# Kernel optimization log

Measured on AMD Instinct MI355X. Metric: run time of the kernel, lower is better.

The kernel has to match this reference:

```python
import jax, jax.numpy as jnp
import numpy as np

PARALLISM = 128          # Subarray[0]
O_BITS = 8               # ADC_resolution
SCALE = float(2 ** O_BITS - 1)          # 255.0
MAXCURRENT = 0.02 * PARALLISM           # 2.56 ; a_scale/w_scale == 2**32-1 so guards skip them


def setup_inputs() -> dict:
    key = jax.random.key(0)
    k1, k2, k3 = jax.random.split(key, 3)
    B, K, N = 8192, 4096, 4096
    x = jax.random.normal(k1, (B, K), dtype=jnp.float32) * 0.1
    weight = jax.random.normal(k2, (N, K), dtype=jnp.float32)  # torch Linear layout [out, in]
    bias = jax.random.normal(k3, (N,), dtype=jnp.float32)
    return {"x": x, "weight": weight, "bias": bias, "layer": 1}


def _quantize_partial(x):
    # output_quantize.forward: clamp to +/-maxcurrent, scale to [−scale, scale], round (STE), rescale
    y = jnp.clip(x, -MAXCURRENT, MAXCURRENT)
    y = y / MAXCURRENT * SCALE
    y = y + jax.lax.stop_gradient(jnp.round(y) - y)  # Round.apply with straight-through grad
    return y / SCALE * MAXCURRENT


def reference(x, weight, bias, layer):
    # Hard_fc: chunked VMM along the input-feature (row) dim with per-subarray ADC quantization
    B, K = x.shape
    w = weight.T                      # [K, N]
    N = w.shape[1]
    num = K // PARALLISM              # K chosen divisible by PARALLISM (32 chunks)
    xc = x.reshape(B, num, PARALLISM).swapaxes(0, 1)       # [num, B, P]
    wc = w.reshape(num, PARALLISM, N)                       # [num, P, N]

    def step(acc, chunk):
        xi, wi = chunk                # [B, P], [P, N]
        return acc + _quantize_partial(xi @ wi), None

    acc0 = jnp.zeros((B, N), dtype=x.dtype)
    out, _ = jax.lax.scan(step, acc0, (xc, wc))
    out = out + bias
    return out.reshape(B, -1)
```

## Files before the change

### kernel.cpp

```cpp
#include <hip/hip_runtime.h>


typedef __attribute__((ext_vector_type(8))) short short8;
typedef __attribute__((ext_vector_type(8))) unsigned short ushort8;
typedef __attribute__((ext_vector_type(4))) float floatx4;

#define BM 128
#define BN 128
#define BK 64

static __device__ __forceinline__ unsigned short f2bf(float f) {
    union { float f; unsigned int u; } v; v.f = f;
    unsigned int u = v.u;
    unsigned int r = (u + 0x7fffu + ((u >> 16) & 1u)) >> 16;
    return (unsigned short)r;
}

__global__ void cast_kernel(const float* __restrict__ in,
                            unsigned short* __restrict__ out,
                            long n8, float s) {
    long i = (long)blockIdx.x * 256 + threadIdx.x;
    const long stride = (long)gridDim.x * 256;
    for (; i < n8; i += stride) {
        float4 a = ((const float4*)in)[2 * i];
        float4 b = ((const float4*)in)[2 * i + 1];
        ushort8 o;
        o[0] = f2bf(a.x * s); o[1] = f2bf(a.y * s);
        o[2] = f2bf(a.z * s); o[3] = f2bf(a.w * s);
        o[4] = f2bf(b.x * s); o[5] = f2bf(b.y * s);
        o[6] = f2bf(b.z * s); o[7] = f2bf(b.w * s);
        ((ushort8*)out)[i] = o;
    }
}

__global__ __launch_bounds__(256, 2) void vmm_kernel(
    const unsigned short* __restrict__ A,
    const unsigned short* __restrict__ Bw,
    const float* __restrict__ bias,
    float* __restrict__ out,
    int N, int K)
{
    __shared__ unsigned short sA[BM * BK];
    __shared__ unsigned short sB[BN * BK];

    const int tid  = threadIdx.x;
    const int wid  = tid >> 6;
    const int lane = tid & 63;

    const int m0 = blockIdx.y * BM;
    const int n0 = blockIdx.x * BN;

    const int waveM = (wid >> 1) * 64;
    const int waveN = (wid & 1) * 64;

    floatx4 acc[4][4];
    floatx4 macc[4][4];
    #pragma unroll
    for (int i = 0; i < 4; ++i)
        #pragma unroll
        for (int j = 0; j < 4; ++j) {
            acc[i][j]  = (floatx4){0.f, 0.f, 0.f, 0.f};
            macc[i][j] = (floatx4){0.f, 0.f, 0.f, 0.f};
        }

    const int srow = lane >> 3;
    const int scol = (((lane & 7) ^ srow) & 7) * 8;

    const unsigned short* gA = A  + (long)m0 * K;
    const unsigned short* gB = Bw + (long)n0 * K;

    for (int k0 = 0; k0 < K; k0 += BK) {
        #pragma unroll
        for (int i = 0; i < 4; ++i) {
            const int seg = i * 4 + wid;
            const long grow = (long)(seg * 8 + srow);
            __builtin_amdgcn_global_load_lds(
                (const __attribute__((address_space(1))) void*)(gA + grow * K + k0 + scol),
                (__attribute__((address_space(3))) void*)(sA + seg * 512),
                16, 0, 0);
            __builtin_amdgcn_global_load_lds(
                (const __attribute__((address_space(1))) void*)(gB + grow * K + k0 + scol),
                (__attribute__((address_space(3))) void*)(sB + seg * 512),
                16, 0, 0);
        }
        __syncthreads();

        #pragma unroll
        for (int kk = 0; kk < BK; kk += 32) {
            const int lc = (kk >> 3) + (lane >> 4);
            const int pc = (lc ^ (lane & 7)) * 8;
            short8 af[4], bfr[4];
            #pragma unroll
            for (int tm = 0; tm < 4; ++tm)
                af[tm] = *(const short8*)(sA + (waveM + tm * 16 + (lane & 15)) * BK + pc);
            #pragma unroll
            for (int tn = 0; tn < 4; ++tn)
                bfr[tn] = *(const short8*)(sB + (waveN + tn * 16 + (lane & 15)) * BK + pc);
            #pragma unroll
            for (int tm = 0; tm < 4; ++tm)
                #pragma unroll
                for (int tn = 0; tn < 4; ++tn)
                    acc[tm][tn] = __builtin_amdgcn_mfma_f32_16x16x32_bf16(
                        af[tm], bfr[tn], acc[tm][tn], 0, 0, 0);
        }

        if (((k0 + BK) & 127) == 0) {
            #pragma unroll
            for (int tm = 0; tm < 4; ++tm)
                #pragma unroll
                for (int tn = 0; tn < 4; ++tn) {
                    #pragma unroll
                    for (int r = 0; r < 4; ++r) {
                        float v = acc[tm][tn][r];
                        v = __builtin_amdgcn_fmed3f(v, -255.0f, 255.0f);
                        v = __builtin_rintf(v);
                        macc[tm][tn][r] += v;
                    }
                    acc[tm][tn] = (floatx4){0.f, 0.f, 0.f, 0.f};
                }
        }
        __syncthreads();
    }

    const float invs = 2.56f / 255.0f;
    #pragma unroll
    for (int tn = 0; tn < 4; ++tn) {
        const int col = n0 + waveN + tn * 16 + (lane & 15);
        const float bv = bias[col];
        #pragma unroll
        for (int tm = 0; tm < 4; ++tm) {
            const int row = m0 + waveM + tm * 16 + (lane >> 4) * 4;
            #pragma unroll
            for (int r = 0; r < 4; ++r)
                out[(long)(row + r) * N + col] = macc[tm][tn][r] * invs + bv;
        }
    }
}

extern "C" void kernel_launch(void* const* d_in, const int* in_sizes, int n_in,
                              void* d_out, int out_size, void* d_ws, size_t ws_size,
                              hipStream_t stream) {
    const float* x    = (const float*)d_in[0];
    const float* w    = (const float*)d_in[1];
    const float* bias = (const float*)d_in[2];

    const int N = in_sizes[2];
    const int K = in_sizes[1] / N;
    const int B = in_sizes[0] / K;
    float* out = (float*)d_out;

    unsigned short* xb = (unsigned short*)d_ws;
    unsigned short* wb = xb + (size_t)B * K;

    cast_kernel<<<2048, 256, 0, stream>>>(x, xb, ((long)B * K) / 8, 1.0f);
    cast_kernel<<<2048, 256, 0, stream>>>(w, wb, ((long)N * K) / 8, 99.609375f);

    dim3 grid(N / BN, B / BM);
    vmm_kernel<<<grid, 256, 0, stream>>>(xb, wb, bias, out, N, K);
}
```

Before: 635.1 us.

## Double-buffer LDS with async global-to-LDS prefetch and widen tile to 128x256

Restructures the GEMM main loop into a software pipeline. LDS is double-buffered, split into 32-wide k sub-slices, and each phase issues the next slice's global_load_lds while running MFMAs on the current one. Manual s_waitcnt/s_barrier replaces the two __syncthreads per iteration, and s_setprio raises priority around the MFMA bursts. The block grows to 512 threads with a 128x256 tile and a new XOR swizzle, which raises LDS use and per-block register pressure and depends on correct vmcnt accounting.

```diff
diff --git a/kernel.cpp b/kernel.cpp
--- a/kernel.cpp
+++ b/kernel.cpp
@@ -6,7 +6,7 @@
 typedef __attribute__((ext_vector_type(4))) float floatx4;
 
 #define BM 128
-#define BN 128
+#define BN 256
 #define BK 64
 
 static __device__ __forceinline__ unsigned short f2bf(float f) {
@@ -33,15 +33,15 @@
     }
 }
 
-__global__ __launch_bounds__(256, 2) void vmm_kernel(
+__global__ __launch_bounds__(512, 2) void vmm_kernel(
     const unsigned short* __restrict__ A,
     const unsigned short* __restrict__ Bw,
     const float* __restrict__ bias,
     float* __restrict__ out,
     int N, int K)
 {
-    __shared__ unsigned short sA[BM * BK];
-    __shared__ unsigned short sB[BN * BK];
+    __shared__ unsigned short sA[2 * BM * BK];
+    __shared__ unsigned short sB[2 * BN * BK];
 
     const int tid  = threadIdx.x;
     const int wid  = tid >> 6;
@@ -50,8 +50,23 @@
     const int m0 = blockIdx.y * BM;
     const int n0 = blockIdx.x * BN;
 
-    const int waveM = (wid >> 1) * 64;
-    const int waveN = (wid & 1) * 64;
+    const int waveM = (wid >> 2) * 64;
+    const int waveN = (wid & 3) * 64;
+
+    const int scl = ((tid & 3) ^ ((tid >> 2) & 3) ^ ((tid >> 4) & 3)) * 8;
+    const unsigned short* srcA  = A  + (long)(m0 + (tid >> 2)) * K + scl;
+    const unsigned short* srcB0 = Bw + (long)(n0 + (tid >> 2)) * K + scl;
+    const unsigned short* srcB1 = srcB0 + (long)128 * K;
+    unsigned short* dA = sA + wid * 512;
+    unsigned short* dB = sB + wid * 512;
+
+    const int cpl = ((lane >> 4) ^ (lane & 3) ^ ((lane >> 2) & 3)) * 8;
+    int aoff[4], boff[4];
+    #pragma unroll
+    for (int t = 0; t < 4; ++t) {
+        aoff[t] = (waveM + t * 16 + (lane & 15)) * 32 + cpl;
+        boff[t] = (waveN + t * 16 + (lane & 15)) * 32 + cpl;
+    }
 
     floatx4 acc[4][4];
     floatx4 macc[4][4];
@@ -63,64 +78,67 @@
             macc[i][j] = (floatx4){0.f, 0.f, 0.f, 0.f};
         }
 
-    const int srow = lane >> 3;
-    const int scol = (((lane & 7) ^ srow) & 7) * 8;
+    #define STAGE(sbuf, kk, sk) do {                                            \
+        __builtin_amdgcn_global_load_lds(                                       \
+            (const __attribute__((address_space(1))) void*)(srcA + (sk) + (kk) * 32), \
+            (__attribute__((address_space(3))) void*)(dA + (sbuf) * 8192 + (kk) * 4096), \
+            16, 0, 0);                                                          \
+        __builtin_amdgcn_global_load_lds(                                       \
+            (const __attribute__((address_space(1))) void*)(srcB0 + (sk) + (kk) * 32), \
+            (__attribute__((address_space(3))) void*)(dB + (sbuf) * 16384 + (kk) * 8192), \
+            16, 0, 0);                                                          \
+        __builtin_amdgcn_global_load_lds(                                       \
+            (const __attribute__((address_space(1))) void*)(srcB1 + (sk) + (kk) * 32), \
+            (__attribute__((address_space(3))) void*)(dB + (sbuf) * 16384 + (kk) * 8192 + 4096), \
+            16, 0, 0);                                                          \
+    } while (0)
 
-    const unsigned short* gA = A  + (long)m0 * K;
-    const unsigned short* gB = Bw + (long)n0 * K;
+    #define PHASE(rbuf, kk, sbuf, sk) do {                                      \
+        asm volatile("s_waitcnt vmcnt(3)\n\ts_barrier" ::: "memory");           \
+        const unsigned short* pa_ = sA + (rbuf) * 8192 + (kk) * 4096;           \
+        const unsigned short* pb_ = sB + (rbuf) * 16384 + (kk) * 8192;          \
+        short8 af_[4], bf_[4];                                                  \
+        _Pragma("unroll")                                                       \
+        for (int t = 0; t < 4; ++t) af_[t] = *(const short8*)(pa_ + aoff[t]);   \
+        _Pragma("unroll")                                                       \
+        for (int t = 0; t < 4; ++t) bf_[t] = *(const short8*)(pb_ + boff[t]);   \
+        STAGE(sbuf, kk, sk);                                                    \
+        __builtin_amdgcn_s_setprio(1);                                          \
+        _Pragma("unroll")                                                       \
+        for (int tm = 0; tm < 4; ++tm)                                          \
+            _Pragma("unroll")                                                   \
+            for (int tn = 0; tn < 4; ++tn)                                      \
+                acc[tm][tn] = __builtin_amdgcn_mfma_f32_16x16x32_bf16(          \
+                    af_[tm], bf_[tn], acc[tm][tn], 0, 0, 0);                    \
+        __builtin_amdgcn_s_setprio(0);                                          \
+    } while (0)
 
-    for (int k0 = 0; k0 < K; k0 += BK) {
-        #pragma unroll
-        for (int i = 0; i < 4; ++i) {
-            const int seg = i * 4 + wid;
-            const long grow = (long)(seg * 8 + srow);
-            __builtin_amdgcn_global_load_lds(
-                (const __attribute__((address_space(1))) void*)(gA + grow * K + k0 + scol),
-                (__attribute__((address_space(3))) void*)(sA + seg * 512),
-                16, 0, 0);
-            __builtin_amdgcn_global_load_lds(
-                (const __attribute__((address_space(1))) void*)(gB + grow * K + k0 + scol),
-                (__attribute__((address_space(3))) void*)(sB + seg * 512),
-                16, 0, 0);
-        }
-        __syncthreads();
+    STAGE(0, 0, 0);
+    STAGE(0, 1, 0);
+
+    for (int k0 = 0; k0 < K; k0 += 128) {
+        const int skA = k0 + 64;
+        const int skB = (k0 + 128 < K) ? (k0 + 128) : 0;
+        PHASE(0, 0, 1, skA);
+        PHASE(0, 1, 1, skA);
+        PHASE(1, 0, 0, skB);
+        PHASE(1, 1, 0, skB);
 
         #pragma unroll
-        for (int kk = 0; kk < BK; kk += 32) {
-            const int lc = (kk >> 3) + (lane >> 4);
-            const int pc = (lc ^ (lane & 7)) * 8;
-            short8 af[4], bfr[4];
+        for (int tm = 0; tm < 4; ++tm)
             #pragma unroll
-            for (int tm = 0; tm < 4; ++tm)
-                af[tm] = *(const short8*)(sA + (waveM + tm * 16 + (lane & 15)) * BK + pc);
-            #pragma unroll
-            for (int tn = 0; tn < 4; ++tn)
-                bfr[tn] = *(const short8*)(sB + (waveN + tn * 16 + (lane & 15)) * BK + pc);
-            #pragma unroll
-            for (int tm = 0; tm < 4; ++tm)
+            for (int tn = 0; tn < 4; ++tn) {
                 #pragma unroll
-                for (int tn = 0; tn < 4; ++tn)
-                    acc[tm][tn] = __builtin_amdgcn_mfma_f32_16x16x32_bf16(
-                        af[tm], bfr[tn], acc[tm][tn], 0, 0, 0);
-        }
-
-        if (((k0 + BK) & 127) == 0) {
-            #pragma unroll
-            for (int tm = 0; tm < 4; ++tm)
-                #pragma unroll
-                for (int tn = 0; tn < 4; ++tn) {
-                    #pragma unroll
-                    for (int r = 0; r < 4; ++r) {
-                        float v = acc[tm][tn][r];
-                        v = __builtin_amdgcn_fmed3f(v, -255.0f, 255.0f);
-                        v = __builtin_rintf(v);
-                        macc[tm][tn][r] += v;
-                    }
-                    acc[tm][tn] = (floatx4){0.f, 0.f, 0.f, 0.f};
+                for (int r = 0; r < 4; ++r) {
+                    float v = acc[tm][tn][r];
+                    v = __builtin_amdgcn_fmed3f(v, -255.0f, 255.0f);
+                    v = __builtin_rintf(v);
+                    macc[tm][tn][r] += v;
                 }
-        }
-        __syncthreads();
+                acc[tm][tn] = (floatx4){0.f, 0.f, 0.f, 0.f};
+            }
     }
+    asm volatile("s_waitcnt vmcnt(0)" ::: "memory");
 
     const float invs = 2.56f / 255.0f;
     #pragma unroll
@@ -135,6 +153,8 @@
                 out[(long)(row + r) * N + col] = macc[tm][tn][r] * invs + bv;
         }
     }
+    #undef PHASE
+    #undef STAGE
 }
 
 extern "C" void kernel_launch(void* const* d_in, const int* in_sizes, int n_in,
@@ -156,5 +176,5 @@
     cast_kernel<<<2048, 256, 0, stream>>>(w, wb, ((long)N * K) / 8, 99.609375f);
 
     dim3 grid(N / BN, B / BM);
-    vmm_kernel<<<grid, 256, 0, stream>>>(xb, wb, bias, out, N, K);
+    vmm_kernel<<<grid, 512, 0, stream>>>(xb, wb, bias, out, N, K);
 }
```

Result: slower. 675.7 us (+6.4%).

## Triple-buffer LDS tiles with async prefetch, widen N tile, swizzle block order

Applied to the files above, without the earlier changes.

Replaces the single-buffered load/sync/compute loop with a three-stage LDS ring. Global-to-LDS loads are issued two iterations ahead and gated with explicit vmcnt waits and a single barrier per iteration, so memory latency overlaps the MFMA work. The N tile doubles to 256 with 512 threads per block. A 1D grid is remapped into grouped tiles for better L2 reuse, and MFMAs run at raised wave priority. LDS use rises to about 144KB per block, which may limit occupancy to one block per CU despite the launch bound of two.

```diff
diff --git a/kernel.cpp b/kernel.cpp
--- a/kernel.cpp
+++ b/kernel.cpp
@@ -6,8 +6,11 @@
 typedef __attribute__((ext_vector_type(4))) float floatx4;
 
 #define BM 128
-#define BN 128
+#define BN 256
 #define BK 64
+
+#define AS1 __attribute__((address_space(1)))
+#define AS3 __attribute__((address_space(3)))
 
 static __device__ __forceinline__ unsigned short f2bf(float f) {
     union { float f; unsigned int u; } v; v.f = f;
@@ -33,25 +36,49 @@
     }
 }
 
-__global__ __launch_bounds__(256, 2) void vmm_kernel(
+__global__ __launch_bounds__(512, 2) void vmm_kernel(
     const unsigned short* __restrict__ A,
     const unsigned short* __restrict__ Bw,
     const float* __restrict__ bias,
     float* __restrict__ out,
     int N, int K)
 {
-    __shared__ unsigned short sA[BM * BK];
-    __shared__ unsigned short sB[BN * BK];
+    __shared__ unsigned short sA[3 * BM * BK];
+    __shared__ unsigned short sB[3 * BN * BK];
 
     const int tid  = threadIdx.x;
     const int wid  = tid >> 6;
     const int lane = tid & 63;
 
-    const int m0 = blockIdx.y * BM;
-    const int n0 = blockIdx.x * BN;
-
-    const int waveM = (wid >> 1) * 64;
-    const int waveN = (wid & 1) * 64;
+    const int ntn = N / BN;
+    int mt, ntile;
+    if (gridDim.x == 1024 && ntn == 16) {
+        const int g   = blockIdx.x & 7;
+        const int idx = blockIdx.x >> 3;
+        mt    = (g << 3) + ((idx >> 2) & 7);
+        ntile = ((idx >> 5) << 2) + (idx & 3);
+    } else {
+        mt = blockIdx.x / ntn;
+        ntile = blockIdx.x - mt * ntn;
+    }
+    const int m0 = mt * BM;
+    const int n0 = ntile * BN;
+
+    const int waveM = (wid >> 2) * 64;
+    const int waveN = (wid & 3) * 64;
+
+    const int r0  = (wid << 3) + (lane >> 3);
+    const int csw = (((lane & 7) ^ (lane >> 3)) << 3);
+    const unsigned short* gA = A  + (long)(m0 + r0) * K + csw;
+    const unsigned short* gB = Bw + (long)(n0 + r0) * K + csw;
+
+    const int c0 = (((lane >> 4) ^ (lane & 7)) << 3);
+    int aoff[4], boff[4];
+    #pragma unroll
+    for (int t = 0; t < 4; ++t) {
+        aoff[t] = (waveM + t * 16 + (lane & 15)) * BK + c0;
+        boff[t] = (waveN + t * 16 + (lane & 15)) * BK + c0;
+    }
 
     floatx4 acc[4][4];
     floatx4 macc[4][4];
@@ -63,48 +90,64 @@
             macc[i][j] = (floatx4){0.f, 0.f, 0.f, 0.f};
         }
 
-    const int srow = lane >> 3;
-    const int scol = (((lane & 7) ^ srow) & 7) * 8;
-
-    const unsigned short* gA = A  + (long)m0 * K;
-    const unsigned short* gB = Bw + (long)n0 * K;
-
-    for (int k0 = 0; k0 < K; k0 += BK) {
-        #pragma unroll
-        for (int i = 0; i < 4; ++i) {
-            const int seg = i * 4 + wid;
-            const long grow = (long)(seg * 8 + srow);
-            __builtin_amdgcn_global_load_lds(
-                (const __attribute__((address_space(1))) void*)(gA + grow * K + k0 + scol),
-                (__attribute__((address_space(3))) void*)(sA + seg * 512),
-                16, 0, 0);
-            __builtin_amdgcn_global_load_lds(
-                (const __attribute__((address_space(1))) void*)(gB + grow * K + k0 + scol),
-                (__attribute__((address_space(3))) void*)(sB + seg * 512),
-                16, 0, 0);
-        }
-        __syncthreads();
-
-        #pragma unroll
-        for (int kk = 0; kk < BK; kk += 32) {
-            const int lc = (kk >> 3) + (lane >> 4);
-            const int pc = (lc ^ (lane & 7)) * 8;
-            short8 af[4], bfr[4];
-            #pragma unroll
-            for (int tm = 0; tm < 4; ++tm)
-                af[tm] = *(const short8*)(sA + (waveM + tm * 16 + (lane & 15)) * BK + pc);
-            #pragma unroll
-            for (int tn = 0; tn < 4; ++tn)
-                bfr[tn] = *(const short8*)(sB + (waveN + tn * 16 + (lane & 15)) * BK + pc);
+    #define STAGE(buf, ksrc) do {                                              \
+        const long ko_ = (ksrc);                                               \
+        __builtin_amdgcn_global_load_lds((const AS1 void*)(gA + ko_),          \
+            (AS3 void*)(sA + (buf) * 8192 + wid * 512), 16, 0, 0);             \
+        __builtin_amdgcn_global_load_lds((const AS1 void*)(gA + 64 * (long)K + ko_), \
+            (AS3 void*)(sA + (buf) * 8192 + 4096 + wid * 512), 16, 0, 0);      \
+        __builtin_amdgcn_global_load_lds((const AS1 void*)(gB + ko_),          \
+            (AS3 void*)(sB + (buf) * 16384 + wid * 512), 16, 0, 0);            \
+        __builtin_amdgcn_global_load_lds((const AS1 void*)(gB + 64 * (long)K + ko_), \
+            (AS3 void*)(sB + (buf) * 16384 + 4096 + wid * 512), 16, 0, 0);     \
+        __builtin_amdgcn_global_load_lds((const AS1 void*)(gB + 128 * (long)K + ko_), \
+            (AS3 void*)(sB + (buf) * 16384 + 8192 + wid * 512), 16, 0, 0);     \
+        __builtin_amdgcn_global_load_lds((const AS1 void*)(gB + 192 * (long)K + ko_), \
+            (AS3 void*)(sB + (buf) * 16384 + 12288 + wid * 512), 16, 0, 0);    \
+    } while (0)
+
+    const int NT = K / BK;
+    STAGE(0, 0);
+    STAGE(1, BK);
+
+    int buf = 0;
+    for (int t = 0; t < NT; ++t) {
+        if (t < NT - 1)
+            asm volatile("s_waitcnt vmcnt(6)\n\ts_barrier" ::: "memory");
+        else
+            asm volatile("s_waitcnt vmcnt(0)\n\ts_barrier" ::: "memory");
+
+        const unsigned short* pa = sA + buf * 8192;
+        const unsigned short* pb = sB + buf * 16384;
+        short8 af[2][4], bfr[2][4];
+        #pragma unroll
+        for (int tm = 0; tm < 4; ++tm) {
+            af[0][tm] = *(const short8*)(pa + aoff[tm]);
+            af[1][tm] = *(const short8*)(pa + (aoff[tm] ^ 32));
+        }
+        #pragma unroll
+        for (int tn = 0; tn < 4; ++tn) {
+            bfr[0][tn] = *(const short8*)(pb + boff[tn]);
+            bfr[1][tn] = *(const short8*)(pb + (boff[tn] ^ 32));
+        }
+
+        if (t + 2 < NT) {
+            const int nb = (buf >= 1) ? buf - 1 : 2;
+            STAGE(nb, (long)(t + 2) * BK);
+        }
+
+        __builtin_amdgcn_s_setprio(1);
+        #pragma unroll
+        for (int h = 0; h < 2; ++h)
             #pragma unroll
             for (int tm = 0; tm < 4; ++tm)
                 #pragma unroll
                 for (int tn = 0; tn < 4; ++tn)
                     acc[tm][tn] = __builtin_amdgcn_mfma_f32_16x16x32_bf16(
-                        af[tm], bfr[tn], acc[tm][tn], 0, 0, 0);
-        }
-
-        if (((k0 + BK) & 127) == 0) {
+                        af[h][tm], bfr[h][tn], acc[tm][tn], 0, 0, 0);
+        __builtin_amdgcn_s_setprio(0);
+
+        if (t & 1) {
             #pragma unroll
             for (int tm = 0; tm < 4; ++tm)
                 #pragma unroll
@@ -119,7 +162,7 @@
                     acc[tm][tn] = (floatx4){0.f, 0.f, 0.f, 0.f};
                 }
         }
-        __syncthreads();
+        buf = (buf == 2) ? 0 : buf + 1;
     }
 
     const float invs = 2.56f / 255.0f;
@@ -135,6 +178,7 @@
                 out[(long)(row + r) * N + col] = macc[tm][tn][r] * invs + bv;
         }
     }
+    #undef STAGE
 }
 
 extern "C" void kernel_launch(void* const* d_in, const int* in_sizes, int n_in,
@@ -155,6 +199,6 @@
     cast_kernel<<<2048, 256, 0, stream>>>(x, xb, ((long)B * K) / 8, 1.0f);
     cast_kernel<<<2048, 256, 0, stream>>>(w, wb, ((long)N * K) / 8, 99.609375f);
 
-    dim3 grid(N / BN, B / BM);
-    vmm_kernel<<<grid, 256, 0, stream>>>(xb, wb, bias, out, N, K);
-}
+    const int nblocks = (N / BN) * (B / BM);
+    vmm_kernel<<<nblocks, 512, 0, stream>>>(xb, wb, bias, out, N, K);
+}
```

After: 593.2 us. -6.6%, faster.
